# Optimization experiments

Hardware: AMD Instinct MI355X
Metric: run time of the kernel (lower is better)

The kernel has to match this reference:

```python
import jax, jax.numpy as jnp
import numpy as np

N_PER_DEG = 30000
MAX_DEG = 6
MIN_DEG = 0
N_ATOMS = N_PER_DEG * (MAX_DEG + 1)  # 210000, atoms sorted by degree
N_FEAT = 128
NB_FILTER = 128
NB_AFFINE = 2 * MAX_DEG + (1 - MIN_DEG)  # 13


def setup_inputs() -> dict:
    key = jax.random.key(0)
    ks = jax.random.split(key, 2 + MAX_DEG)
    atoms = jax.random.normal(ks[0], (N_ATOMS, N_FEAT), dtype=jnp.float32)
    # glorot-ish scale for the 13 affine weights
    W = jax.random.normal(ks[1], (NB_AFFINE, N_FEAT, NB_FILTER), dtype=jnp.float32) * (1.0 / np.sqrt(N_FEAT))
    b = jnp.zeros((NB_AFFINE, NB_FILTER), dtype=jnp.float32)
    # deg_slice[d] = (start, count) for degree d in 0..MAX_DEG; equal-size buckets
    deg_slice = jnp.asarray(
        np.stack([np.arange(MAX_DEG + 1) * N_PER_DEG,
                  np.full(MAX_DEG + 1, N_PER_DEG)], axis=1).astype(np.int32))
    inp = {"atoms": atoms, "W": W, "b": b, "deg_slice": deg_slice}
    for d in range(1, MAX_DEG + 1):
        inp[f"adj{d}"] = jax.random.randint(ks[1 + d], (N_PER_DEG, d), 0, N_ATOMS, dtype=jnp.int32)
    return inp


def reference(atoms, W, b, deg_slice, adj1, adj2, adj3, adj4, adj5, adj6):
    """Degree-bucketed graph convolution (deepchem GraphConv, linear activation).

    W ordering matches the original iterator: for deg=1..MAX_DEG the pair
    (rel=W[2*(deg-1)], self=W[2*(deg-1)+1]), then deg-0 self uses W[2*MAX_DEG].
    Output concat order: deg 0 bucket first, then deg 1..MAX_DEG.
    """
    adjs = [adj1, adj2, adj3, adj4, adj5, adj6]
    ds = np.asarray(deg_slice)  # structural constant: static slice bounds
    outs = [None] * (MAX_DEG + 1 - MIN_DEG)
    # deg 0: self-affine only
    s0, c0 = int(ds[0, 0]), int(ds[0, 1])
    outs[0] = atoms[s0:s0 + c0] @ W[2 * MAX_DEG] + b[2 * MAX_DEG]
    for deg in range(1, MAX_DEG + 1):
        s, c = int(ds[deg, 0]), int(ds[deg, 1])
        # gather neighbors of each degree-deg atom and sum: (c, deg, F) -> (c, F)
        rel = jnp.take(atoms, adjs[deg - 1], axis=0).sum(axis=1)
        out = (rel @ W[2 * (deg - 1)] + b[2 * (deg - 1)]
               + atoms[s:s + c] @ W[2 * (deg - 1) + 1] + b[2 * (deg - 1) + 1])
        outs[deg] = out
    return jnp.concatenate(outs, axis=0)  # (N_ATOMS, NB_FILTER)
```

## Files before the change

kernel.cpp:

```cpp
#include <hip/hip_runtime.h>
#include <hip/hip_bf16.h>

#define NPD 30000
#define NF  128
#define MAXDEG 6
#define LDK2 264

typedef __attribute__((ext_vector_type(8))) short short8;
typedef __attribute__((ext_vector_type(4))) float floatx4;

__device__ __forceinline__ unsigned short f2bf(float f) {
    __hip_bfloat16 h = __float2bfloat16(f);
    return __builtin_bit_cast(unsigned short, h);
}
__device__ __forceinline__ uint4 pack16B(float4 a, float4 b) {
    uint4 v;
    v.x = (unsigned)f2bf(a.x) | ((unsigned)f2bf(a.y) << 16);
    v.y = (unsigned)f2bf(a.z) | ((unsigned)f2bf(a.w) << 16);
    v.z = (unsigned)f2bf(b.x) | ((unsigned)f2bf(b.y) << 16);
    v.w = (unsigned)f2bf(b.z) | ((unsigned)f2bf(b.w) << 16);
    return v;
}

__device__ __forceinline__ void wt_tile(const float* __restrict__ W,
                                        unsigned short* __restrict__ Wt,
                                        int bx, unsigned short (*t)[33]) {
    const int a  = bx >> 4;
    const int k0 = ((bx >> 2) & 3) * 32, n0 = (bx & 3) * 32;
    const int tx = threadIdx.x & 31, ty = threadIdx.x >> 5;
    const float*    Wp  = W  + (size_t)a * NF * NF;
    unsigned short* Wtp = Wt + (size_t)a * NF * NF;
#pragma unroll
    for (int i = 0; i < 32; i += 8)
        t[ty + i][tx] = f2bf(Wp[(size_t)(k0 + ty + i) * NF + (n0 + tx)]);
    __syncthreads();
#pragma unroll
    for (int i = 0; i < 32; i += 8)
        Wtp[(size_t)(n0 + ty + i) * NF + (k0 + tx)] = t[tx][ty + i];
}

template <int DEG>
__device__ __forceinline__ void gather_work(const float* __restrict__ atoms,
                                            const int* __restrict__ adj,
                                            unsigned short* __restrict__ relbuf) {
    const int t = threadIdx.x;
    const int r = blockIdx.x * 32 + (t >> 3);
    if (r >= NPD) return;
    const int c = (t & 7) * 16;
    const int* arow = adj + (size_t)r * DEG;
    int idxs[DEG];
#pragma unroll
    for (int j = 0; j < DEG; ++j) idxs[j] = arow[j];
    float s[16];
#pragma unroll
    for (int i = 0; i < 16; ++i) s[i] = 0.f;
#pragma unroll
    for (int j = 0; j < DEG; ++j) {
        const float4* p = (const float4*)(atoms + (size_t)idxs[j] * NF + c);
        float4 q0 = p[0], q1 = p[1], q2 = p[2], q3 = p[3];
        s[0]  += q0.x; s[1]  += q0.y; s[2]  += q0.z; s[3]  += q0.w;
        s[4]  += q1.x; s[5]  += q1.y; s[6]  += q1.z; s[7]  += q1.w;
        s[8]  += q2.x; s[9]  += q2.y; s[10] += q2.z; s[11] += q2.w;
        s[12] += q3.x; s[13] += q3.y; s[14] += q3.z; s[15] += q3.w;
    }
    uint4 w0 = pack16B(make_float4(s[0], s[1], s[2], s[3]),
                       make_float4(s[4], s[5], s[6], s[7]));
    uint4 w1 = pack16B(make_float4(s[8], s[9], s[10], s[11]),
                       make_float4(s[12], s[13], s[14], s[15]));
    unsigned short* op = relbuf + ((size_t)(DEG - 1) * NPD + r) * NF + c;
    *(uint4*)op       = w0;
    *(uint4*)(op + 8) = w1;
}

__global__ __launch_bounds__(256) void gather_kernel(
    const float* __restrict__ atoms, const float* __restrict__ W,
    unsigned short* __restrict__ Wt,
    const int* __restrict__ adj1, const int* __restrict__ adj2,
    const int* __restrict__ adj3, const int* __restrict__ adj4,
    const int* __restrict__ adj5, const int* __restrict__ adj6,
    unsigned short* __restrict__ relbuf)
{
    __shared__ unsigned short t[32][33];
    if (blockIdx.y == 6) {
        if (blockIdx.x < 208) wt_tile(W, Wt, blockIdx.x, t);
        return;
    }
    switch (blockIdx.y) {
        case 0: gather_work<1>(atoms, adj1, relbuf); break;
        case 1: gather_work<2>(atoms, adj2, relbuf); break;
        case 2: gather_work<3>(atoms, adj3, relbuf); break;
        case 3: gather_work<4>(atoms, adj4, relbuf); break;
        case 4: gather_work<5>(atoms, adj5, relbuf); break;
        default: gather_work<6>(atoms, adj6, relbuf); break;
    }
}

template <int DEG>
__device__ __forceinline__ void gemm_work(
    const float* __restrict__ atomsF, const unsigned short* __restrict__ relbuf,
    const unsigned short* __restrict__ Wt, const float* __restrict__ bvec,
    float* __restrict__ out, unsigned short* __restrict__ sA)
{
    const int tid  = threadIdx.x;
    const int lane = tid & 63, wave = tid >> 6;
    const int nb = lane & 15;
    const int kq = (lane >> 4) * 8;
    const int col0 = wave * 32;
    const int row0_local = blockIdx.x * 32;
    const int valid = min(32, NPD - row0_local);
    const int row0g = DEG * NPD + row0_local;
    const int wi_self = (DEG == 0) ? 12 : (2 * DEG - 1);
    const int wi_rel  = (DEG > 0) ? 2 * (DEG - 1) : 0;

    floatx4 acc[2][2];
#pragma unroll
    for (int i = 0; i < 2; i++)
#pragma unroll
        for (int j = 0; j < 2; j++) acc[i][j] = (floatx4){0.f, 0.f, 0.f, 0.f};

#pragma unroll
    for (int p = 0; p < 2; ++p) {
        int idx = p * 256 + tid;
        int r = idx >> 4, ch = (idx & 15) * 8;
        int rr = min(r, valid - 1);
        const float4* pf = (const float4*)(atomsF + (size_t)(row0g + rr) * NF + ch);
        *(uint4*)&sA[r * LDK2 + ch] = pack16B(pf[0], pf[1]);
    }
    if constexpr (DEG > 0) {
#pragma unroll
        for (int p = 0; p < 2; ++p) {
            int idx = p * 256 + tid;
            int r = idx >> 4, ch = (idx & 15) * 8;
            int rr = min(r, valid - 1);
            *(uint4*)&sA[r * LDK2 + NF + ch] =
                *(const uint4*)(relbuf + ((size_t)(DEG - 1) * NPD + row0_local + rr) * NF + ch);
        }
    }
    __syncthreads();

    constexpr int NKK = (DEG > 0) ? 8 : 4;
#pragma unroll
    for (int kk = 0; kk < NKK; ++kk) {
        const int wi = (kk < 4) ? wi_self : wi_rel;
        const unsigned short* Wp = Wt + (size_t)wi * NF * NF;
        short8 bfr[2];
#pragma unroll
        for (int nt = 0; nt < 2; ++nt)
            bfr[nt] = *(const short8*)(Wp + (size_t)(col0 + nt * 16 + nb) * NF
                                          + (kk & 3) * 32 + kq);
        short8 af[2];
#pragma unroll
        for (int mt = 0; mt < 2; ++mt)
            af[mt] = *(const short8*)&sA[(mt * 16 + nb) * LDK2 + kk * 32 + kq];
#pragma unroll
        for (int mt = 0; mt < 2; ++mt)
#pragma unroll
            for (int nt = 0; nt < 2; ++nt)
                acc[mt][nt] = __builtin_amdgcn_mfma_f32_16x16x32_bf16(
                    af[mt], bfr[nt], acc[mt][nt], 0, 0, 0);
    }

    float bias[2];
#pragma unroll
    for (int nt = 0; nt < 2; ++nt) {
        const int n = col0 + nt * 16 + nb;
        float bv = bvec[wi_self * NF + n];
        if (DEG > 0) bv += bvec[wi_rel * NF + n];
        bias[nt] = bv;
    }
    const int rq = (lane >> 4) * 4;
#pragma unroll
    for (int mt = 0; mt < 2; ++mt) {
#pragma unroll
        for (int reg = 0; reg < 4; ++reg) {
            const int r = mt * 16 + rq + reg;
            if (r < valid) {
                float* op = out + (size_t)(row0g + r) * NF;
#pragma unroll
                for (int nt = 0; nt < 2; ++nt)
                    op[col0 + nt * 16 + nb] = acc[mt][nt][reg] + bias[nt];
            }
        }
    }
}

__global__ __launch_bounds__(256) void gemm_kernel(
    const float* __restrict__ atomsF, const unsigned short* __restrict__ relbuf,
    const unsigned short* __restrict__ Wt, const float* __restrict__ bvec,
    float* __restrict__ out)
{
    __shared__ unsigned short sA[32 * LDK2];
    switch (blockIdx.y) {
        case 0: gemm_work<0>(atomsF, relbuf, Wt, bvec, out, sA); break;
        case 1: gemm_work<1>(atomsF, relbuf, Wt, bvec, out, sA); break;
        case 2: gemm_work<2>(atomsF, relbuf, Wt, bvec, out, sA); break;
        case 3: gemm_work<3>(atomsF, relbuf, Wt, bvec, out, sA); break;
        case 4: gemm_work<4>(atomsF, relbuf, Wt, bvec, out, sA); break;
        case 5: gemm_work<5>(atomsF, relbuf, Wt, bvec, out, sA); break;
        default: gemm_work<6>(atomsF, relbuf, Wt, bvec, out, sA); break;
    }
}

__global__ __launch_bounds__(128) void naive_kernel(
    const float* __restrict__ atoms, const float* __restrict__ W,
    const float* __restrict__ b,
    const int* __restrict__ adj1, const int* __restrict__ adj2,
    const int* __restrict__ adj3, const int* __restrict__ adj4,
    const int* __restrict__ adj5, const int* __restrict__ adj6,
    float* __restrict__ out)
{
    const int i = blockIdx.x;
    const int deg = i / NPD, r = i - deg * NPD, n = threadIdx.x;
    __shared__ float selfr[NF], relr[NF];
    selfr[n] = atoms[(size_t)i * NF + n];
    float rv = 0.f;
    if (deg > 0) {
        const int* adjs[6] = {adj1, adj2, adj3, adj4, adj5, adj6};
        const int* adj = adjs[deg - 1];
        for (int j = 0; j < deg; ++j)
            rv += atoms[(size_t)adj[(size_t)r * deg + j] * NF + n];
    }
    relr[n] = rv;
    __syncthreads();
    const int ws  = (deg == 0) ? 12 : 2 * deg - 1;
    const int wrl = 2 * (deg - 1);
    float acc = b[ws * NF + n] + ((deg > 0) ? b[wrl * NF + n] : 0.f);
    for (int k = 0; k < NF; ++k) {
        acc += selfr[k] * W[(size_t)ws * NF * NF + (size_t)k * NF + n];
        if (deg > 0) acc += relr[k] * W[(size_t)wrl * NF * NF + (size_t)k * NF + n];
    }
    out[(size_t)i * NF + n] = acc;
}

extern "C" void kernel_launch(void* const* d_in, const int* in_sizes, int n_in,
                              void* d_out, int out_size, void* d_ws, size_t ws_size,
                              hipStream_t stream) {
    const float* atoms = (const float*)d_in[0];
    const float* W     = (const float*)d_in[1];
    const float* b     = (const float*)d_in[2];
    const int* adj1 = (const int*)d_in[4];
    const int* adj2 = (const int*)d_in[5];
    const int* adj3 = (const int*)d_in[6];
    const int* adj4 = (const int*)d_in[7];
    const int* adj5 = (const int*)d_in[8];
    const int* adj6 = (const int*)d_in[9];

    const size_t wt_bytes  = (size_t)13 * NF * NF * sizeof(unsigned short);
    const size_t rel_bytes = (size_t)6 * NPD * NF * sizeof(unsigned short);

    if (ws_size >= wt_bytes + rel_bytes) {
        unsigned short* Wt     = (unsigned short*)d_ws;
        unsigned short* relbuf = (unsigned short*)((char*)d_ws + wt_bytes);
        const int gx = (NPD + 31) / 32;
        gather_kernel<<<dim3(gx, 7), 256, 0, stream>>>(
            atoms, W, Wt, adj1, adj2, adj3, adj4, adj5, adj6, relbuf);
        gemm_kernel<<<dim3(gx, 7), 256, 0, stream>>>(atoms, relbuf, Wt, b,
                                                     (float*)d_out);
    } else {
        naive_kernel<<<NPD * (MAXDEG + 1), NF, 0, stream>>>(
            atoms, W, b, adj1, adj2, adj3, adj4, adj5, adj6, (float*)d_out);
    }
}
```

Measured before the change: 299.5 us.

## Fuse neighbor gather into GEMM kernel, drop relbuf round-trip

Result: faster. 269.6 us (-10.0%).

```diff
diff --git a/kernel.cpp b/kernel.cpp
--- a/kernel.cpp
+++ b/kernel.cpp
@@ -22,9 +22,10 @@
     return v;
 }
 
-__device__ __forceinline__ void wt_tile(const float* __restrict__ W,
-                                        unsigned short* __restrict__ Wt,
-                                        int bx, unsigned short (*t)[33]) {
+__global__ __launch_bounds__(256) void wt_kernel(const float* __restrict__ W,
+                                                 unsigned short* __restrict__ Wt) {
+    __shared__ unsigned short t[32][33];
+    const int bx = blockIdx.x;
     const int a  = bx >> 4;
     const int k0 = ((bx >> 2) & 3) * 32, n0 = (bx & 3) * 32;
     const int tx = threadIdx.x & 31, ty = threadIdx.x >> 5;
@@ -40,65 +41,9 @@
 }
 
 template <int DEG>
-__device__ __forceinline__ void gather_work(const float* __restrict__ atoms,
-                                            const int* __restrict__ adj,
-                                            unsigned short* __restrict__ relbuf) {
-    const int t = threadIdx.x;
-    const int r = blockIdx.x * 32 + (t >> 3);
-    if (r >= NPD) return;
-    const int c = (t & 7) * 16;
-    const int* arow = adj + (size_t)r * DEG;
-    int idxs[DEG];
-#pragma unroll
-    for (int j = 0; j < DEG; ++j) idxs[j] = arow[j];
-    float s[16];
-#pragma unroll
-    for (int i = 0; i < 16; ++i) s[i] = 0.f;
-#pragma unroll
-    for (int j = 0; j < DEG; ++j) {
-        const float4* p = (const float4*)(atoms + (size_t)idxs[j] * NF + c);
-        float4 q0 = p[0], q1 = p[1], q2 = p[2], q3 = p[3];
-        s[0]  += q0.x; s[1]  += q0.y; s[2]  += q0.z; s[3]  += q0.w;
-        s[4]  += q1.x; s[5]  += q1.y; s[6]  += q1.z; s[7]  += q1.w;
-        s[8]  += q2.x; s[9]  += q2.y; s[10] += q2.z; s[11] += q2.w;
-        s[12] += q3.x; s[13] += q3.y; s[14] += q3.z; s[15] += q3.w;
-    }
-    uint4 w0 = pack16B(make_float4(s[0], s[1], s[2], s[3]),
-                       make_float4(s[4], s[5], s[6], s[7]));
-    uint4 w1 = pack16B(make_float4(s[8], s[9], s[10], s[11]),
-                       make_float4(s[12], s[13], s[14], s[15]));
-    unsigned short* op = relbuf + ((size_t)(DEG - 1) * NPD + r) * NF + c;
-    *(uint4*)op       = w0;
-    *(uint4*)(op + 8) = w1;
-}
-
-__global__ __launch_bounds__(256) void gather_kernel(
-    const float* __restrict__ atoms, const float* __restrict__ W,
-    unsigned short* __restrict__ Wt,
-    const int* __restrict__ adj1, const int* __restrict__ adj2,
-    const int* __restrict__ adj3, const int* __restrict__ adj4,
-    const int* __restrict__ adj5, const int* __restrict__ adj6,
-    unsigned short* __restrict__ relbuf)
-{
-    __shared__ unsigned short t[32][33];
-    if (blockIdx.y == 6) {
-        if (blockIdx.x < 208) wt_tile(W, Wt, blockIdx.x, t);
-        return;
-    }
-    switch (blockIdx.y) {
-        case 0: gather_work<1>(atoms, adj1, relbuf); break;
-        case 1: gather_work<2>(atoms, adj2, relbuf); break;
-        case 2: gather_work<3>(atoms, adj3, relbuf); break;
-        case 3: gather_work<4>(atoms, adj4, relbuf); break;
-        case 4: gather_work<5>(atoms, adj5, relbuf); break;
-        default: gather_work<6>(atoms, adj6, relbuf); break;
-    }
-}
-
-template <int DEG>
-__device__ __forceinline__ void gemm_work(
-    const float* __restrict__ atomsF, const unsigned short* __restrict__ relbuf,
-    const unsigned short* __restrict__ Wt, const float* __restrict__ bvec,
+__device__ __forceinline__ void fused_work(
+    const float* __restrict__ atoms, const unsigned short* __restrict__ Wt,
+    const float* __restrict__ bvec, const int* __restrict__ adj,
     float* __restrict__ out, unsigned short* __restrict__ sA)
 {
     const int tid  = threadIdx.x;
@@ -106,37 +51,68 @@
     const int nb = lane & 15;
     const int kq = (lane >> 4) * 8;
     const int col0 = wave * 32;
-    const int row0_local = blockIdx.x * 32;
-    const int valid = min(32, NPD - row0_local);
-    const int row0g = DEG * NPD + row0_local;
+    const int row0 = blockIdx.x * 32;
+    const int valid = min(32, NPD - row0);
+    const int row0g = DEG * NPD + row0;
     const int wi_self = (DEG == 0) ? 12 : (2 * DEG - 1);
     const int wi_rel  = (DEG > 0) ? 2 * (DEG - 1) : 0;
 
+    const int r0 = tid >> 4,          ch0 = (tid & 15) * 8;
+    const int r1 = (tid >> 4) + 16,   ch1 = ch0;
+    const int rr0 = min(r0, valid - 1), rr1 = min(r1, valid - 1);
+    const float4* sp0 = (const float4*)(atoms + (size_t)(row0g + rr0) * NF + ch0);
+    const float4* sp1 = (const float4*)(atoms + (size_t)(row0g + rr1) * NF + ch1);
+    float4 sv0 = sp0[0], sv1 = sp0[1], sv2 = sp1[0], sv3 = sp1[1];
+
+    if constexpr (DEG > 0) {
+        const int gr  = tid >> 3;
+        const int gc  = (tid & 7) * 16;
+        const int grr = min(gr, valid - 1);
+        const int* arow = adj + (size_t)(row0 + grr) * DEG;
+        int idxs[DEG];
+#pragma unroll
+        for (int j = 0; j < DEG; ++j) idxs[j] = arow[j];
+
+        *(uint4*)&sA[r0 * LDK2 + ch0] = pack16B(sv0, sv1);
+        *(uint4*)&sA[r1 * LDK2 + ch1] = pack16B(sv2, sv3);
+
+        float s[16];
+#pragma unroll
+        for (int i = 0; i < 16; ++i) s[i] = 0.f;
+        float4 q0, q1, q2, q3, n0, n1, n2, n3;
+        {
+            const float4* p = (const float4*)(atoms + (size_t)idxs[0] * NF + gc);
+            q0 = p[0]; q1 = p[1]; q2 = p[2]; q3 = p[3];
+        }
+#pragma unroll
+        for (int j = 0; j < DEG; ++j) {
+            if (j + 1 < DEG) {
+                const float4* p = (const float4*)(atoms + (size_t)idxs[j + 1] * NF + gc);
+                n0 = p[0]; n1 = p[1]; n2 = p[2]; n3 = p[3];
+            }
+            s[0]  += q0.x; s[1]  += q0.y; s[2]  += q0.z; s[3]  += q0.w;
+            s[4]  += q1.x; s[5]  += q1.y; s[6]  += q1.z; s[7]  += q1.w;
+            s[8]  += q2.x; s[9]  += q2.y; s[10] += q2.z; s[11] += q2.w;
+            s[12] += q3.x; s[13] += q3.y; s[14] += q3.z; s[15] += q3.w;
+            q0 = n0; q1 = n1; q2 = n2; q3 = n3;
+        }
+        uint4 w0 = pack16B(make_float4(s[0], s[1], s[2], s[3]),
+                           make_float4(s[4], s[5], s[6], s[7]));
+        uint4 w1 = pack16B(make_float4(s[8], s[9], s[10], s[11]),
+                           make_float4(s[12], s[13], s[14], s[15]));
+        *(uint4*)&sA[gr * LDK2 + NF + gc]     = w0;
+        *(uint4*)&sA[gr * LDK2 + NF + gc + 8] = w1;
+    } else {
+        *(uint4*)&sA[r0 * LDK2 + ch0] = pack16B(sv0, sv1);
+        *(uint4*)&sA[r1 * LDK2 + ch1] = pack16B(sv2, sv3);
+    }
+    __syncthreads();
+
     floatx4 acc[2][2];
 #pragma unroll
     for (int i = 0; i < 2; i++)
 #pragma unroll
         for (int j = 0; j < 2; j++) acc[i][j] = (floatx4){0.f, 0.f, 0.f, 0.f};
-
-#pragma unroll
-    for (int p = 0; p < 2; ++p) {
-        int idx = p * 256 + tid;
-        int r = idx >> 4, ch = (idx & 15) * 8;
-        int rr = min(r, valid - 1);
-        const float4* pf = (const float4*)(atomsF + (size_t)(row0g + rr) * NF + ch);
-        *(uint4*)&sA[r * LDK2 + ch] = pack16B(pf[0], pf[1]);
-    }
-    if constexpr (DEG > 0) {
-#pragma unroll
-        for (int p = 0; p < 2; ++p) {
-            int idx = p * 256 + tid;
-            int r = idx >> 4, ch = (idx & 15) * 8;
-            int rr = min(r, valid - 1);
-            *(uint4*)&sA[r * LDK2 + NF + ch] =
-                *(const uint4*)(relbuf + ((size_t)(DEG - 1) * NPD + row0_local + rr) * NF + ch);
-        }
-    }
-    __syncthreads();
 
     constexpr int NKK = (DEG > 0) ? 8 : 4;
 #pragma unroll
@@ -178,26 +154,30 @@
                 float* op = out + (size_t)(row0g + r) * NF;
 #pragma unroll
                 for (int nt = 0; nt < 2; ++nt)
-                    op[col0 + nt * 16 + nb] = acc[mt][nt][reg] + bias[nt];
+                    __builtin_nontemporal_store(acc[mt][nt][reg] + bias[nt],
+                                                op + col0 + nt * 16 + nb);
             }
         }
     }
 }
 
-__global__ __launch_bounds__(256) void gemm_kernel(
-    const float* __restrict__ atomsF, const unsigned short* __restrict__ relbuf,
-    const unsigned short* __restrict__ Wt, const float* __restrict__ bvec,
+__global__ __launch_bounds__(256) void fused_kernel(
+    const float* __restrict__ atoms, const unsigned short* __restrict__ Wt,
+    const float* __restrict__ bvec,
+    const int* __restrict__ adj1, const int* __restrict__ adj2,
+    const int* __restrict__ adj3, const int* __restrict__ adj4,
+    const int* __restrict__ adj5, const int* __restrict__ adj6,
     float* __restrict__ out)
 {
     __shared__ unsigned short sA[32 * LDK2];
     switch (blockIdx.y) {
-        case 0: gemm_work<0>(atomsF, relbuf, Wt, bvec, out, sA); break;
-        case 1: gemm_work<1>(atomsF, relbuf, Wt, bvec, out, sA); break;
-        case 2: gemm_work<2>(atomsF, relbuf, Wt, bvec, out, sA); break;
-        case 3: gemm_work<3>(atomsF, relbuf, Wt, bvec, out, sA); break;
-        case 4: gemm_work<4>(atomsF, relbuf, Wt, bvec, out, sA); break;
-        case 5: gemm_work<5>(atomsF, relbuf, Wt, bvec, out, sA); break;
-        default: gemm_work<6>(atomsF, relbuf, Wt, bvec, out, sA); break;
+        case 0: fused_work<0>(atoms, Wt, bvec, nullptr, out, sA); break;
+        case 1: fused_work<1>(atoms, Wt, bvec, adj1,    out, sA); break;
+        case 2: fused_work<2>(atoms, Wt, bvec, adj2,    out, sA); break;
+        case 3: fused_work<3>(atoms, Wt, bvec, adj3,    out, sA); break;
+        case 4: fused_work<4>(atoms, Wt, bvec, adj4,    out, sA); break;
+        case 5: fused_work<5>(atoms, Wt, bvec, adj5,    out, sA); break;
+        default: fused_work<6>(atoms, Wt, bvec, adj6,   out, sA); break;
     }
 }
 
@@ -245,17 +225,14 @@
     const int* adj5 = (const int*)d_in[8];
     const int* adj6 = (const int*)d_in[9];
 
-    const size_t wt_bytes  = (size_t)13 * NF * NF * sizeof(unsigned short);
-    const size_t rel_bytes = (size_t)6 * NPD * NF * sizeof(unsigned short);
-
-    if (ws_size >= wt_bytes + rel_bytes) {
-        unsigned short* Wt     = (unsigned short*)d_ws;
-        unsigned short* relbuf = (unsigned short*)((char*)d_ws + wt_bytes);
+    const size_t wt_bytes = (size_t)13 * NF * NF * sizeof(unsigned short);
+
+    if (ws_size >= wt_bytes) {
+        unsigned short* Wt = (unsigned short*)d_ws;
+        wt_kernel<<<208, 256, 0, stream>>>(W, Wt);
         const int gx = (NPD + 31) / 32;
-        gather_kernel<<<dim3(gx, 7), 256, 0, stream>>>(
-            atoms, W, Wt, adj1, adj2, adj3, adj4, adj5, adj6, relbuf);
-        gemm_kernel<<<dim3(gx, 7), 256, 0, stream>>>(atoms, relbuf, Wt, b,
-                                                     (float*)d_out);
+        fused_kernel<<<dim3(gx, 7), 256, 0, stream>>>(
+            atoms, Wt, b, adj1, adj2, adj3, adj4, adj5, adj6, (float*)d_out);
     } else {
         naive_kernel<<<NPD * (MAXDEG + 1), NF, 0, stream>>>(
             atoms, W, b, adj1, adj2, adj3, adj4, adj5, adj6, (float*)d_out);
```
